# Kernel optimization log

Hardware: AMD Instinct MI355X
Metric: run time of the kernel (lower is better)

## Reference

```python
import jax, jax.numpy as jnp
import numpy as np

N = 100000      # nodes
E = 1_000_000   # edges (avg degree ~10)
D_IN = 64
HID = 64
N_CLS = 32


def setup_inputs() -> dict:
    key = jax.random.key(0)
    ks = jax.random.split(key, 9)
    x = jax.random.normal(ks[0], (N, D_IN), dtype=jnp.float32)
    edge_index = jax.random.randint(ks[1], (2, E), 0, N, dtype=jnp.int32)
    s_in = 1.0 / np.sqrt(D_IN)
    s_h = 1.0 / np.sqrt(HID)
    W1 = jax.random.normal(ks[2], (D_IN, HID), dtype=jnp.float32) * s_in
    b1 = jnp.zeros((HID,), dtype=jnp.float32)
    W2 = jax.random.normal(ks[3], (HID, HID), dtype=jnp.float32) * s_h
    b2 = jnp.zeros((HID,), dtype=jnp.float32)
    Wl = jax.random.normal(ks[4], (HID, N_CLS), dtype=jnp.float32) * s_h
    bl = jnp.zeros((N_CLS,), dtype=jnp.float32)
    return {"x": x, "edge_index": edge_index,
            "W1": W1, "b1": b1, "W2": W2, "b2": b2, "Wl": Wl, "bl": bl}


def reference(x, edge_index, W1, b1, W2, b2, Wl, bl):
    # GCNConv default: add self-loops, symmetric normalization D^-1/2 (A+I) D^-1/2
    loop = jnp.arange(N, dtype=edge_index.dtype)
    src = jnp.concatenate([edge_index[0], loop])  # [E+N]
    dst = jnp.concatenate([edge_index[1], loop])  # [E+N]

    deg = jax.ops.segment_sum(jnp.ones_like(dst, dtype=jnp.float32), dst,
                              num_segments=N)              # [N]
    dinv = jnp.where(deg > 0, jax.lax.rsqrt(deg), 0.0)      # D^-1/2
    norm = dinv[src] * dinv[dst]                            # [E+N]

    def gcn_conv(h, W, b):
        h = h @ W                                           # [N, F_out]
        msg = h[src] * norm[:, None]                        # gather + scale
        return jax.ops.segment_sum(msg, dst, num_segments=N) + b

    h = jax.nn.relu(gcn_conv(x, W1, b1))
    h = jax.nn.relu(gcn_conv(h, W2, b2))
    return h @ Wl + bl
```

## Files before the change

kernel.cpp:

```cpp
#include <hip/hip_runtime.h>
#include <hip/hip_fp16.h>
#include <math.h>


#define TPB    256
#define EBLKS  256
#define BSH    9
#define BNODES (1 << BSH)

__global__ __launch_bounds__(TPB)
void k_p1hist(const int* __restrict__ dst, int* __restrict__ OFS,
              int E, int CH, int NBC) {
    __shared__ int h[512];
    int tid = threadIdx.x, b = blockIdx.x;
    for (int i = tid; i < NBC; i += TPB) h[i] = 0;
    __syncthreads();
    int beg = b * CH, end = min(E, beg + CH);
    if (beg < end) {
        int nfull = (end - beg) & ~3;
        for (int i = beg + tid * 4; i < beg + nfull; i += TPB * 4) {
            int4 d = *(const int4*)&dst[i];
            atomicAdd(&h[d.x >> BSH], 1);
            atomicAdd(&h[d.y >> BSH], 1);
            atomicAdd(&h[d.z >> BSH], 1);
            atomicAdd(&h[d.w >> BSH], 1);
        }
        if (tid < (end - beg) - nfull)
            atomicAdd(&h[dst[beg + nfull + tid] >> BSH], 1);
    }
    __syncthreads();
    for (int c = tid; c < NBC; c += TPB) OFS[c * EBLKS + b] = h[c];
}

__global__ __launch_bounds__(TPB)
void k_scanA(const int* __restrict__ OFS, int* __restrict__ bsum, int total) {
    __shared__ int s[TPB];
    int tid = threadIdx.x;
    int i0  = blockIdx.x * 1024 + tid * 4;
    int t = 0;
#pragma unroll
    for (int k = 0; k < 4; ++k) {
        int i = i0 + k;
        t += (i < total) ? OFS[i] : 0;
    }
    s[tid] = t;
    __syncthreads();
    for (int off = TPB / 2; off > 0; off >>= 1) {
        if (tid < off) s[tid] += s[tid + off];
        __syncthreads();
    }
    if (tid == 0) bsum[blockIdx.x] = s[0];
}

__global__ __launch_bounds__(TPB)
void k_scanC(int* __restrict__ OFS, const int* __restrict__ bsum,
             int NBLK, int total) {
    __shared__ int s[TPB];
    __shared__ int pfx;
    int tid = threadIdx.x;
    if (tid < 64) {
        int v = (tid < NBLK && tid < (int)blockIdx.x) ? bsum[tid] : 0;
#pragma unroll
        for (int off = 1; off < 64; off <<= 1) v += __shfl_xor(v, off);
        if (tid == 0) pfx = v;
    }
    int i0 = blockIdx.x * 1024 + tid * 4;
    int v[4];
#pragma unroll
    for (int k = 0; k < 4; ++k) {
        int i = i0 + k;
        v[k] = (i < total) ? OFS[i] : 0;
    }
    int tsum = v[0] + v[1] + v[2] + v[3];
    s[tid] = tsum;
    __syncthreads();
    for (int off = 1; off < TPB; off <<= 1) {
        int x = (tid >= off) ? s[tid - off] : 0;
        __syncthreads();
        s[tid] += x;
        __syncthreads();
    }
    int base = pfx + (s[tid] - tsum);
#pragma unroll
    for (int k = 0; k < 4; ++k) {
        int i = i0 + k;
        if (i < total) {
            OFS[i] = base;
            base += v[k];
        }
    }
}

__global__ __launch_bounds__(TPB)
void k_p1scatter(const int* __restrict__ src, const int* __restrict__ dst,
                 const int* __restrict__ OFS, int* __restrict__ ebuf,
                 int E, int CH, int NBC) {
    __shared__ int cur[512];
    int tid = threadIdx.x, b = blockIdx.x;
    for (int c = tid; c < NBC; c += TPB) cur[c] = OFS[c * EBLKS + b];
    __syncthreads();
    int beg = b * CH, end = min(E, beg + CH);
    if (beg >= end) return;
    int nfull = (end - beg) & ~3;
    for (int i = beg + tid * 4; i < beg + nfull; i += TPB * 4) {
        int4 s4 = *(const int4*)&src[i];
        int4 d4 = *(const int4*)&dst[i];
        int p0 = atomicAdd(&cur[d4.x >> BSH], 1);
        int p1 = atomicAdd(&cur[d4.y >> BSH], 1);
        int p2 = atomicAdd(&cur[d4.z >> BSH], 1);
        int p3 = atomicAdd(&cur[d4.w >> BSH], 1);
        ebuf[p0] = (s4.x << BSH) | (d4.x & (BNODES - 1));
        ebuf[p1] = (s4.y << BSH) | (d4.y & (BNODES - 1));
        ebuf[p2] = (s4.z << BSH) | (d4.z & (BNODES - 1));
        ebuf[p3] = (s4.w << BSH) | (d4.w & (BNODES - 1));
    }
    if (tid < (end - beg) - nfull) {
        int i = beg + nfull + tid;
        int d = dst[i];
        int p = atomicAdd(&cur[d >> BSH], 1);
        ebuf[p] = (src[i] << BSH) | (d & (BNODES - 1));
    }
}

__global__ __launch_bounds__(TPB)
void k_p2(const int* __restrict__ ebuf, const int* __restrict__ OFS,
          int* __restrict__ row_ptr, float* __restrict__ dinv,
          int* __restrict__ colw, int N, int E, int NBC) {
    __shared__ int cnt[BNODES];
    __shared__ int ofs[BNODES];
    __shared__ int s1[TPB];
    int tid = threadIdx.x, c = blockIdx.x;
    int beg = OFS[c * EBLKS];
    int end = (c == NBC - 1) ? E : OFS[(c + 1) * EBLKS];
    for (int i = tid; i < BNODES; i += TPB) cnt[i] = 0;
    __syncthreads();
    for (int i = beg + tid; i < end; i += TPB)
        atomicAdd(&cnt[ebuf[i] & (BNODES - 1)], 1);
    __syncthreads();
    int a0 = cnt[2 * tid], a1 = cnt[2 * tid + 1];
    int pairsum = a0 + a1;
    s1[tid] = pairsum;
    __syncthreads();
    for (int off = 1; off < TPB; off <<= 1) {
        int x = (tid >= off) ? s1[tid - off] : 0;
        __syncthreads();
        s1[tid] += x;
        __syncthreads();
    }
    int ex = s1[tid] - pairsum;
    int node0 = (c << BSH) + 2 * tid;
    ofs[2 * tid]     = beg + ex;
    ofs[2 * tid + 1] = beg + ex + a0;
    if (node0 < N) {
        row_ptr[node0] = beg + ex;
        dinv[node0]    = rsqrtf((float)(a0 + 1));
    }
    if (node0 + 1 < N) {
        row_ptr[node0 + 1] = beg + ex + a0;
        dinv[node0 + 1]    = rsqrtf((float)(a1 + 1));
    }
    if (c == NBC - 1 && tid == 0) row_ptr[N] = E;
    cnt[2 * tid] = 0;
    cnt[2 * tid + 1] = 0;
    __syncthreads();
    for (int i0 = beg + tid; i0 < end; i0 += TPB * 4) {
        int sv[4], dl[4], pos[4];
        int have = 0;
#pragma unroll
        for (int k = 0; k < 4; ++k) {
            int i = i0 + k * TPB;
            if (i < end) {
                int e = ebuf[i];
                sv[k] = e >> BSH;
                dl[k] = e & (BNODES - 1);
                have = k + 1;
            }
        }
#pragma unroll
        for (int k = 0; k < 4; ++k) {
            if (k < have) {
                int r  = atomicAdd(&cnt[dl[k]], 1);
                pos[k] = ofs[dl[k]] + r;
            }
        }
#pragma unroll
        for (int k = 0; k < 4; ++k)
            if (k < have) colw[pos[k]] = sv[k];
    }
}

template <int F, bool FINAL, bool HIN>
__launch_bounds__(256)
__global__ void k_mm(const void* __restrict__ in, const float* __restrict__ W,
                     const float* __restrict__ bias, const float* __restrict__ dinv,
                     void* __restrict__ out, int n) {
    __shared__ float in_s[64 * 68];
    __shared__ float w_s[64 * F];

    const int tid  = threadIdx.x;
    const int row0 = blockIdx.x * 64;

    for (int i4 = tid; i4 < (64 * F) / 4; i4 += 256)
        ((float4*)w_s)[i4] = ((const float4*)W)[i4];

    if constexpr (HIN) {
        for (int idx = tid; idx < 64 * 8; idx += 256) {
            int r  = idx >> 3;
            int c8 = idx & 7;
            uint4 u = make_uint4(0u, 0u, 0u, 0u);
            if (row0 + r < n)
                u = *(const uint4*)((const __half*)in + (size_t)(row0 + r) * 64 + c8 * 8);
            float2 f0 = __half22float2(*(__half2*)&u.x);
            float2 f1 = __half22float2(*(__half2*)&u.y);
            float2 f2 = __half22float2(*(__half2*)&u.z);
            float2 f3 = __half22float2(*(__half2*)&u.w);
            float* o = &in_s[r * 68 + c8 * 8];
            *(float4*)&o[0] = make_float4(f0.x, f0.y, f1.x, f1.y);
            *(float4*)&o[4] = make_float4(f2.x, f2.y, f3.x, f3.y);
        }
    } else {
        for (int idx = tid; idx < 64 * 16; idx += 256) {
            int r  = idx >> 4;
            int c4 = idx & 15;
            float4 v;
            if (row0 + r < n)
                v = *(const float4*)((const float*)in + (size_t)(row0 + r) * 64 + c4 * 4);
            else
                v = make_float4(0.f, 0.f, 0.f, 0.f);
            *(float4*)&in_s[r * 68 + c4 * 4] = v;
        }
    }
    __syncthreads();

    constexpr int CPT = F / 16;
    const int tx = tid & 15;
    const int ty = tid >> 4;

    float acc[4][CPT];
#pragma unroll
    for (int r = 0; r < 4; ++r)
#pragma unroll
        for (int c = 0; c < CPT; ++c) acc[r][c] = 0.f;

#pragma unroll 4
    for (int k = 0; k < 64; ++k) {
        float b[CPT];
#pragma unroll
        for (int c = 0; c < CPT; ++c) b[c] = w_s[k * F + tx * CPT + c];
#pragma unroll
        for (int r = 0; r < 4; ++r) {
            float a = in_s[(ty * 4 + r) * 68 + k];
#pragma unroll
            for (int c = 0; c < CPT; ++c) acc[r][c] = fmaf(a, b[c], acc[r][c]);
        }
    }

#pragma unroll
    for (int r = 0; r < 4; ++r) {
        int row = row0 + ty * 4 + r;
        if (row >= n) continue;
        if constexpr (FINAL) {
#pragma unroll
            for (int c = 0; c < CPT; ++c) {
                int col = tx * CPT + c;
                ((float*)out)[(size_t)row * F + col] = acc[r][c] + bias[col];
            }
        } else {
            float dd = dinv[row];
            __half2 p0 = __floats2half2_rn(acc[r][0] * dd, acc[r][1] * dd);
            __half2 p1 = __floats2half2_rn(acc[r][2] * dd, acc[r][3] * dd);
            uint2 u = make_uint2(*(unsigned*)&p0, *(unsigned*)&p1);
            *(uint2*)((__half*)out + (size_t)row * 64 + tx * 4) = u;
        }
    }
    if constexpr (!FINAL) {
        if (blockIdx.x == 0 && tid < 16)
            *(uint2*)((__half*)out + (size_t)n * 64 + tid * 4) = make_uint2(0u, 0u);
    }
}

__global__ __launch_bounds__(256)
void k_gather(const int* __restrict__ row_ptr, const int* __restrict__ colw,
              const float* __restrict__ dinv, const float* __restrict__ bias,
              const __half* __restrict__ t, __half* __restrict__ agg, int N) {
    int tid  = threadIdx.x;
    int wv   = tid >> 6;
    int lane = tid & 63;
    int g = lane >> 3;
    int p = lane & 7;
    int d = blockIdx.x * 32 + wv * 8 + g;

    int beg = 0, end = 0;
    if (d < N) { beg = row_ptr[d]; end = row_ptr[d + 1]; }

    float acc[8];
#pragma unroll
    for (int k = 0; k < 8; ++k) acc[k] = 0.f;

    for (int e = beg; e < end; e += 2) {
        int s0 = colw[e];
        int s1 = (e + 1 < end) ? colw[e + 1] : N;
        uint4 a0 = *(const uint4*)(t + (size_t)s0 * 64 + p * 8);
        uint4 a1 = *(const uint4*)(t + (size_t)s1 * 64 + p * 8);
        float2 f;
        f = __half22float2(*(__half2*)&a0.x); acc[0] += f.x; acc[1] += f.y;
        f = __half22float2(*(__half2*)&a0.y); acc[2] += f.x; acc[3] += f.y;
        f = __half22float2(*(__half2*)&a0.z); acc[4] += f.x; acc[5] += f.y;
        f = __half22float2(*(__half2*)&a0.w); acc[6] += f.x; acc[7] += f.y;
        f = __half22float2(*(__half2*)&a1.x); acc[0] += f.x; acc[1] += f.y;
        f = __half22float2(*(__half2*)&a1.y); acc[2] += f.x; acc[3] += f.y;
        f = __half22float2(*(__half2*)&a1.z); acc[4] += f.x; acc[5] += f.y;
        f = __half22float2(*(__half2*)&a1.w); acc[6] += f.x; acc[7] += f.y;
    }

    if (d < N) {
        float dd = dinv[d];
        uint4 a = *(const uint4*)(t + (size_t)d * 64 + p * 8);
        float4 b0 = *(const float4*)&bias[p * 8];
        float4 b1 = *(const float4*)&bias[p * 8 + 4];
        float2 s0 = __half22float2(*(__half2*)&a.x);
        float2 s1 = __half22float2(*(__half2*)&a.y);
        float2 s2 = __half22float2(*(__half2*)&a.z);
        float2 s3 = __half22float2(*(__half2*)&a.w);
        float o0 = fmaxf(fmaf(dd, acc[0] + s0.x, b0.x), 0.f);
        float o1 = fmaxf(fmaf(dd, acc[1] + s0.y, b0.y), 0.f);
        float o2 = fmaxf(fmaf(dd, acc[2] + s1.x, b0.z), 0.f);
        float o3 = fmaxf(fmaf(dd, acc[3] + s1.y, b0.w), 0.f);
        float o4 = fmaxf(fmaf(dd, acc[4] + s2.x, b1.x), 0.f);
        float o5 = fmaxf(fmaf(dd, acc[5] + s2.y, b1.y), 0.f);
        float o6 = fmaxf(fmaf(dd, acc[6] + s3.x, b1.z), 0.f);
        float o7 = fmaxf(fmaf(dd, acc[7] + s3.y, b1.w), 0.f);
        __half2 h0 = __floats2half2_rn(o0, o1);
        __half2 h1 = __floats2half2_rn(o2, o3);
        __half2 h2 = __floats2half2_rn(o4, o5);
        __half2 h3 = __floats2half2_rn(o6, o7);
        uint4 u = make_uint4(*(unsigned*)&h0, *(unsigned*)&h1,
                             *(unsigned*)&h2, *(unsigned*)&h3);
        *(uint4*)(agg + (size_t)d * 64 + p * 8) = u;
    }
}

extern "C" void kernel_launch(void* const* d_in, const int* in_sizes, int n_in,
                              void* d_out, int out_size, void* d_ws, size_t ws_size,
                              hipStream_t stream) {
    const float* x  = (const float*)d_in[0];
    const int*   ei = (const int*)d_in[1];
    const float* W1 = (const float*)d_in[2];
    const float* b1 = (const float*)d_in[3];
    const float* W2 = (const float*)d_in[4];
    const float* b2 = (const float*)d_in[5];
    const float* Wl = (const float*)d_in[6];
    const float* bl = (const float*)d_in[7];
    float*       out = (float*)d_out;

    const int N = in_sizes[0] / 64;
    const int E = in_sizes[1] / 2;
    const int* srcp = ei;
    const int* dstp = ei + E;

    const int NBC   = (N + BNODES - 1) / BNODES;
    const int CH    = (((E + EBLKS - 1) / EBLKS) + 3) & ~3;
    const int total = NBC * EBLKS;
    const int NBLK  = (total + 1023) / 1024;

    char*  ws  = (char*)d_ws;
    size_t off = 0;
    auto alloc = [&](size_t bytes) -> void* {
        void* p = (void*)(ws + off);
        off += (bytes + 255) & ~(size_t)255;
        return p;
    };
    int*    OFS     = (int*)alloc(((size_t)total + 1) * 4);
    int*    bsum    = (int*)alloc((size_t)NBLK * 4);
    int*    ebuf    = (int*)alloc((size_t)E * 4);
    int*    row_ptr = (int*)alloc((size_t)(N + 1) * 4);
    float*  dinv    = (float*)alloc((size_t)N * 4);
    int*    colw    = (int*)alloc((size_t)E * 4);
    __half* t1      = (__half*)alloc((size_t)(N + 1) * 64 * 2);
    __half* agg1    = (__half*)alloc((size_t)N * 64 * 2);
    __half* t2      = t1;
    __half* agg2    = agg1;

    const int nb_mm = (N + 63) / 64;
    const int nb_g  = (N + 31) / 32;

    k_p1hist   <<<EBLKS, TPB, 0, stream>>>(dstp, OFS, E, CH, NBC);
    k_scanA    <<<NBLK,  TPB, 0, stream>>>(OFS, bsum, total);
    k_scanC    <<<NBLK,  TPB, 0, stream>>>(OFS, bsum, NBLK, total);
    k_p1scatter<<<EBLKS, TPB, 0, stream>>>(srcp, dstp, OFS, ebuf, E, CH, NBC);
    k_p2       <<<NBC,   TPB, 0, stream>>>(ebuf, OFS, row_ptr, dinv, colw, N, E, NBC);

    k_mm<64, false, false><<<nb_mm, 256, 0, stream>>>(x, W1, nullptr, dinv, t1, N);
    k_gather<<<nb_g, 256, 0, stream>>>(row_ptr, colw, dinv, b1, t1, agg1, N);

    k_mm<64, false, true><<<nb_mm, 256, 0, stream>>>(agg1, W2, nullptr, dinv, t2, N);
    k_gather<<<nb_g, 256, 0, stream>>>(row_ptr, colw, dinv, b2, t2, agg2, N);

    k_mm<32, true, true><<<nb_mm, 256, 0, stream>>>(agg2, Wl, bl, nullptr, out, N);
}
```

Measured before the change: 209.7 us.

## Degree-sort nodes within buckets for gather load balance and unroll edges by four

k_p2 now builds a per-bucket permutation that orders destination nodes by in-degree (counting sort with 64 bins), and k_gather processes nodes in that order so that the 8 node-groups sharing a wavefront have similar edge counts, cutting divergence from the variable-length edge loops. The gather inner loop is also unrolled from 2 to 4 edges per iteration, giving more independent loads in flight. Costs are an extra perm array, an indirection load per node, scattered output writes, and more padding loads for short rows.

Result: slower. 218.8 us (+4.4%).

```diff
diff --git a/kernel.cpp b/kernel.cpp
--- a/kernel.cpp
+++ b/kernel.cpp
@@ -125,10 +125,13 @@
 __global__ __launch_bounds__(TPB)
 void k_p2(const int* __restrict__ ebuf, const int* __restrict__ OFS,
           int* __restrict__ row_ptr, float* __restrict__ dinv,
-          int* __restrict__ colw, int N, int E, int NBC) {
+          int* __restrict__ colw, int* __restrict__ perm,
+          int N, int E, int NBC) {
     __shared__ int cnt[BNODES];
     __shared__ int ofs[BNODES];
     __shared__ int s1[TPB];
+    __shared__ int dh[64];
+    __shared__ int db[64];
     int tid = threadIdx.x, c = blockIdx.x;
     int beg = OFS[c * EBLKS];
     int end = (c == NBC - 1) ? E : OFS[(c + 1) * EBLKS];
@@ -148,21 +151,43 @@
         __syncthreads();
     }
     int ex = s1[tid] - pairsum;
-    int node0 = (c << BSH) + 2 * tid;
+    int cbase = c << BSH;
+    int node0 = cbase + 2 * tid;
+    bool has0 = node0 < N, has1 = node0 + 1 < N;
     ofs[2 * tid]     = beg + ex;
     ofs[2 * tid + 1] = beg + ex + a0;
-    if (node0 < N) {
+    if (has0) {
         row_ptr[node0] = beg + ex;
         dinv[node0]    = rsqrtf((float)(a0 + 1));
     }
-    if (node0 + 1 < N) {
+    if (has1) {
         row_ptr[node0 + 1] = beg + ex + a0;
         dinv[node0 + 1]    = rsqrtf((float)(a1 + 1));
     }
     if (c == NBC - 1 && tid == 0) row_ptr[N] = E;
+
+    if (tid < 64) dh[tid] = 0;
     cnt[2 * tid] = 0;
     cnt[2 * tid + 1] = 0;
     __syncthreads();
+    int b0 = min(a0, 63), b1 = min(a1, 63);
+    if (has0) atomicAdd(&dh[b0], 1);
+    if (has1) atomicAdd(&dh[b1], 1);
+    __syncthreads();
+    if (tid < 64) {
+        int v = dh[tid];
+        int incl = v;
+#pragma unroll
+        for (int o = 1; o < 64; o <<= 1) {
+            int x = __shfl_up(incl, o);
+            if ((tid & 63) >= o) incl += x;
+        }
+        db[tid] = incl - v;
+    }
+    __syncthreads();
+    if (has0) { int r = atomicAdd(&db[b0], 1); perm[cbase + r] = node0; }
+    if (has1) { int r = atomicAdd(&db[b1], 1); perm[cbase + r] = node0 + 1; }
+
     for (int i0 = beg + tid; i0 < end; i0 += TPB * 4) {
         int sv[4], dl[4], pos[4];
         int have = 0;
@@ -281,6 +306,7 @@
 
 __global__ __launch_bounds__(256)
 void k_gather(const int* __restrict__ row_ptr, const int* __restrict__ colw,
+              const int* __restrict__ perm,
               const float* __restrict__ dinv, const float* __restrict__ bias,
               const __half* __restrict__ t, __half* __restrict__ agg, int N) {
     int tid  = threadIdx.x;
@@ -288,20 +314,28 @@
     int lane = tid & 63;
     int g = lane >> 3;
     int p = lane & 7;
-    int d = blockIdx.x * 32 + wv * 8 + g;
-
-    int beg = 0, end = 0;
-    if (d < N) { beg = row_ptr[d]; end = row_ptr[d + 1]; }
+    int idx = blockIdx.x * 32 + wv * 8 + g;
+
+    int d = 0, beg = 0, end = 0;
+    if (idx < N) {
+        d   = perm[idx];
+        beg = row_ptr[d];
+        end = row_ptr[d + 1];
+    }
 
     float acc[8];
 #pragma unroll
     for (int k = 0; k < 8; ++k) acc[k] = 0.f;
 
-    for (int e = beg; e < end; e += 2) {
+    for (int e = beg; e < end; e += 4) {
         int s0 = colw[e];
         int s1 = (e + 1 < end) ? colw[e + 1] : N;
+        int s2 = (e + 2 < end) ? colw[e + 2] : N;
+        int s3 = (e + 3 < end) ? colw[e + 3] : N;
         uint4 a0 = *(const uint4*)(t + (size_t)s0 * 64 + p * 8);
         uint4 a1 = *(const uint4*)(t + (size_t)s1 * 64 + p * 8);
+        uint4 a2 = *(const uint4*)(t + (size_t)s2 * 64 + p * 8);
+        uint4 a3 = *(const uint4*)(t + (size_t)s3 * 64 + p * 8);
         float2 f;
         f = __half22float2(*(__half2*)&a0.x); acc[0] += f.x; acc[1] += f.y;
         f = __half22float2(*(__half2*)&a0.y); acc[2] += f.x; acc[3] += f.y;
@@ -311,9 +345,17 @@
         f = __half22float2(*(__half2*)&a1.y); acc[2] += f.x; acc[3] += f.y;
         f = __half22float2(*(__half2*)&a1.z); acc[4] += f.x; acc[5] += f.y;
         f = __half22float2(*(__half2*)&a1.w); acc[6] += f.x; acc[7] += f.y;
-    }
-
-    if (d < N) {
+        f = __half22float2(*(__half2*)&a2.x); acc[0] += f.x; acc[1] += f.y;
+        f = __half22float2(*(__half2*)&a2.y); acc[2] += f.x; acc[3] += f.y;
+        f = __half22float2(*(__half2*)&a2.z); acc[4] += f.x; acc[5] += f.y;
+        f = __half22float2(*(__half2*)&a2.w); acc[6] += f.x; acc[7] += f.y;
+        f = __half22float2(*(__half2*)&a3.x); acc[0] += f.x; acc[1] += f.y;
+        f = __half22float2(*(__half2*)&a3.y); acc[2] += f.x; acc[3] += f.y;
+        f = __half22float2(*(__half2*)&a3.z); acc[4] += f.x; acc[5] += f.y;
+        f = __half22float2(*(__half2*)&a3.w); acc[6] += f.x; acc[7] += f.y;
+    }
+
+    if (idx < N) {
         float dd = dinv[d];
         uint4 a = *(const uint4*)(t + (size_t)d * 64 + p * 8);
         float4 b0 = *(const float4*)&bias[p * 8];
@@ -376,6 +418,7 @@
     int*    row_ptr = (int*)alloc((size_t)(N + 1) * 4);
     float*  dinv    = (float*)alloc((size_t)N * 4);
     int*    colw    = (int*)alloc((size_t)E * 4);
+    int*    perm    = (int*)alloc((size_t)N * 4);
     __half* t1      = (__half*)alloc((size_t)(N + 1) * 64 * 2);
     __half* agg1    = (__half*)alloc((size_t)N * 64 * 2);
     __half* t2      = t1;
@@ -388,13 +431,13 @@
     k_scanA    <<<NBLK,  TPB, 0, stream>>>(OFS, bsum, total);
     k_scanC    <<<NBLK,  TPB, 0, stream>>>(OFS, bsum, NBLK, total);
     k_p1scatter<<<EBLKS, TPB, 0, stream>>>(srcp, dstp, OFS, ebuf, E, CH, NBC);
-    k_p2       <<<NBC,   TPB, 0, stream>>>(ebuf, OFS, row_ptr, dinv, colw, N, E, NBC);
+    k_p2       <<<NBC,   TPB, 0, stream>>>(ebuf, OFS, row_ptr, dinv, colw, perm, N, E, NBC);
 
     k_mm<64, false, false><<<nb_mm, 256, 0, stream>>>(x, W1, nullptr, dinv, t1, N);
-    k_gather<<<nb_g, 256, 0, stream>>>(row_ptr, colw, dinv, b1, t1, agg1, N);
+    k_gather<<<nb_g, 256, 0, stream>>>(row_ptr, colw, perm, dinv, b1, t1, agg1, N);
 
     k_mm<64, false, true><<<nb_mm, 256, 0, stream>>>(agg1, W2, nullptr, dinv, t2, N);
-    k_gather<<<nb_g, 256, 0, stream>>>(row_ptr, colw, dinv, b2, t2, agg2, N);
+    k_gather<<<nb_g, 256, 0, stream>>>(row_ptr, colw, perm, dinv, b2, t2, agg2, N);
 
     k_mm<32, true, true><<<nb_mm, 256, 0, stream>>>(agg2, Wl, bl, nullptr, out, N);
 }
```

## Shrink CSR buckets to 128 nodes, widen binning blocks, unroll gather by four

Applied to the files above, without the earlier changes.

The bucket shift drops from 9 to 7, so each counting-sort bucket covers 128 nodes and there are about 782 of them. The histogram and scatter kernels move to 1024 threads with larger shared tables, and the second pass now maps one thread per node. The scan prefix loop is generalised so it works with more than 64 partial sums. The gather loop now issues four neighbour row loads per iteration instead of two, to get more memory requests in flight. In exchange, the second pass leaves half its threads idle, there are more scan blocks, and register pressure in the gather rises.

Result: faster. 201.1 us (-4.1%).

```diff
diff --git a/kernel.cpp b/kernel.cpp
--- a/kernel.cpp
+++ b/kernel.cpp
@@ -4,21 +4,22 @@
 
 
 #define TPB    256
+#define TPB1   1024
 #define EBLKS  256
-#define BSH    9
+#define BSH    7
 #define BNODES (1 << BSH)
 
-__global__ __launch_bounds__(TPB)
+__global__ __launch_bounds__(TPB1)
 void k_p1hist(const int* __restrict__ dst, int* __restrict__ OFS,
               int E, int CH, int NBC) {
-    __shared__ int h[512];
+    __shared__ int h[1024];
     int tid = threadIdx.x, b = blockIdx.x;
-    for (int i = tid; i < NBC; i += TPB) h[i] = 0;
+    h[tid] = 0;
     __syncthreads();
     int beg = b * CH, end = min(E, beg + CH);
     if (beg < end) {
         int nfull = (end - beg) & ~3;
-        for (int i = beg + tid * 4; i < beg + nfull; i += TPB * 4) {
+        for (int i = beg + tid * 4; i < beg + nfull; i += TPB1 * 4) {
             int4 d = *(const int4*)&dst[i];
             atomicAdd(&h[d.x >> BSH], 1);
             atomicAdd(&h[d.y >> BSH], 1);
@@ -29,7 +30,7 @@
             atomicAdd(&h[dst[beg + nfull + tid] >> BSH], 1);
     }
     __syncthreads();
-    for (int c = tid; c < NBC; c += TPB) OFS[c * EBLKS + b] = h[c];
+    for (int c = tid; c < NBC; c += TPB1) OFS[c * EBLKS + b] = h[c];
 }
 
 __global__ __launch_bounds__(TPB)
@@ -53,13 +54,13 @@
 }
 
 __global__ __launch_bounds__(TPB)
-void k_scanC(int* __restrict__ OFS, const int* __restrict__ bsum,
-             int NBLK, int total) {
+void k_scanC(int* __restrict__ OFS, const int* __restrict__ bsum, int total) {
     __shared__ int s[TPB];
     __shared__ int pfx;
     int tid = threadIdx.x;
     if (tid < 64) {
-        int v = (tid < NBLK && tid < (int)blockIdx.x) ? bsum[tid] : 0;
+        int v = 0;
+        for (int j = tid; j < (int)blockIdx.x; j += 64) v += bsum[j];
 #pragma unroll
         for (int off = 1; off < 64; off <<= 1) v += __shfl_xor(v, off);
         if (tid == 0) pfx = v;
@@ -91,18 +92,18 @@
     }
 }
 
-__global__ __launch_bounds__(TPB)
+__global__ __launch_bounds__(TPB1)
 void k_p1scatter(const int* __restrict__ src, const int* __restrict__ dst,
                  const int* __restrict__ OFS, int* __restrict__ ebuf,
                  int E, int CH, int NBC) {
-    __shared__ int cur[512];
+    __shared__ int cur[1024];
     int tid = threadIdx.x, b = blockIdx.x;
-    for (int c = tid; c < NBC; c += TPB) cur[c] = OFS[c * EBLKS + b];
+    for (int c = tid; c < NBC; c += TPB1) cur[c] = OFS[c * EBLKS + b];
     __syncthreads();
     int beg = b * CH, end = min(E, beg + CH);
     if (beg >= end) return;
     int nfull = (end - beg) & ~3;
-    for (int i = beg + tid * 4; i < beg + nfull; i += TPB * 4) {
+    for (int i = beg + tid * 4; i < beg + nfull; i += TPB1 * 4) {
         int4 s4 = *(const int4*)&src[i];
         int4 d4 = *(const int4*)&dst[i];
         int p0 = atomicAdd(&cur[d4.x >> BSH], 1);
@@ -132,14 +133,13 @@
     int tid = threadIdx.x, c = blockIdx.x;
     int beg = OFS[c * EBLKS];
     int end = (c == NBC - 1) ? E : OFS[(c + 1) * EBLKS];
-    for (int i = tid; i < BNODES; i += TPB) cnt[i] = 0;
+    if (tid < BNODES) cnt[tid] = 0;
     __syncthreads();
     for (int i = beg + tid; i < end; i += TPB)
         atomicAdd(&cnt[ebuf[i] & (BNODES - 1)], 1);
     __syncthreads();
-    int a0 = cnt[2 * tid], a1 = cnt[2 * tid + 1];
-    int pairsum = a0 + a1;
-    s1[tid] = pairsum;
+    int a = (tid < BNODES) ? cnt[tid] : 0;
+    s1[tid] = a;
     __syncthreads();
     for (int off = 1; off < TPB; off <<= 1) {
         int x = (tid >= off) ? s1[tid - off] : 0;
@@ -147,21 +147,17 @@
         s1[tid] += x;
         __syncthreads();
     }
-    int ex = s1[tid] - pairsum;
-    int node0 = (c << BSH) + 2 * tid;
-    ofs[2 * tid]     = beg + ex;
-    ofs[2 * tid + 1] = beg + ex + a0;
-    if (node0 < N) {
-        row_ptr[node0] = beg + ex;
-        dinv[node0]    = rsqrtf((float)(a0 + 1));
-    }
-    if (node0 + 1 < N) {
-        row_ptr[node0 + 1] = beg + ex + a0;
-        dinv[node0 + 1]    = rsqrtf((float)(a1 + 1));
+    int ex = s1[tid] - a;
+    if (tid < BNODES) {
+        int node = (c << BSH) + tid;
+        ofs[tid] = beg + ex;
+        if (node < N) {
+            row_ptr[node] = beg + ex;
+            dinv[node]    = rsqrtf((float)(a + 1));
+        }
+        cnt[tid] = 0;
     }
     if (c == NBC - 1 && tid == 0) row_ptr[N] = E;
-    cnt[2 * tid] = 0;
-    cnt[2 * tid + 1] = 0;
     __syncthreads();
     for (int i0 = beg + tid; i0 < end; i0 += TPB * 4) {
         int sv[4], dl[4], pos[4];
@@ -297,11 +293,15 @@
 #pragma unroll
     for (int k = 0; k < 8; ++k) acc[k] = 0.f;
 
-    for (int e = beg; e < end; e += 2) {
+    for (int e = beg; e < end; e += 4) {
         int s0 = colw[e];
         int s1 = (e + 1 < end) ? colw[e + 1] : N;
+        int s2 = (e + 2 < end) ? colw[e + 2] : N;
+        int s3 = (e + 3 < end) ? colw[e + 3] : N;
         uint4 a0 = *(const uint4*)(t + (size_t)s0 * 64 + p * 8);
         uint4 a1 = *(const uint4*)(t + (size_t)s1 * 64 + p * 8);
+        uint4 a2 = *(const uint4*)(t + (size_t)s2 * 64 + p * 8);
+        uint4 a3 = *(const uint4*)(t + (size_t)s3 * 64 + p * 8);
         float2 f;
         f = __half22float2(*(__half2*)&a0.x); acc[0] += f.x; acc[1] += f.y;
         f = __half22float2(*(__half2*)&a0.y); acc[2] += f.x; acc[3] += f.y;
@@ -311,6 +311,14 @@
         f = __half22float2(*(__half2*)&a1.y); acc[2] += f.x; acc[3] += f.y;
         f = __half22float2(*(__half2*)&a1.z); acc[4] += f.x; acc[5] += f.y;
         f = __half22float2(*(__half2*)&a1.w); acc[6] += f.x; acc[7] += f.y;
+        f = __half22float2(*(__half2*)&a2.x); acc[0] += f.x; acc[1] += f.y;
+        f = __half22float2(*(__half2*)&a2.y); acc[2] += f.x; acc[3] += f.y;
+        f = __half22float2(*(__half2*)&a2.z); acc[4] += f.x; acc[5] += f.y;
+        f = __half22float2(*(__half2*)&a2.w); acc[6] += f.x; acc[7] += f.y;
+        f = __half22float2(*(__half2*)&a3.x); acc[0] += f.x; acc[1] += f.y;
+        f = __half22float2(*(__half2*)&a3.y); acc[2] += f.x; acc[3] += f.y;
+        f = __half22float2(*(__half2*)&a3.z); acc[4] += f.x; acc[5] += f.y;
+        f = __half22float2(*(__half2*)&a3.w); acc[6] += f.x; acc[7] += f.y;
     }
 
     if (d < N) {
@@ -384,11 +392,11 @@
     const int nb_mm = (N + 63) / 64;
     const int nb_g  = (N + 31) / 32;
 
-    k_p1hist   <<<EBLKS, TPB, 0, stream>>>(dstp, OFS, E, CH, NBC);
-    k_scanA    <<<NBLK,  TPB, 0, stream>>>(OFS, bsum, total);
-    k_scanC    <<<NBLK,  TPB, 0, stream>>>(OFS, bsum, NBLK, total);
-    k_p1scatter<<<EBLKS, TPB, 0, stream>>>(srcp, dstp, OFS, ebuf, E, CH, NBC);
-    k_p2       <<<NBC,   TPB, 0, stream>>>(ebuf, OFS, row_ptr, dinv, colw, N, E, NBC);
+    k_p1hist   <<<EBLKS, TPB1, 0, stream>>>(dstp, OFS, E, CH, NBC);
+    k_scanA    <<<NBLK,  TPB,  0, stream>>>(OFS, bsum, total);
+    k_scanC    <<<NBLK,  TPB,  0, stream>>>(OFS, bsum, total);
+    k_p1scatter<<<EBLKS, TPB1, 0, stream>>>(srcp, dstp, OFS, ebuf, E, CH, NBC);
+    k_p2       <<<NBC,   TPB,  0, stream>>>(ebuf, OFS, row_ptr, dinv, colw, N, E, NBC);
 
     k_mm<64, false, false><<<nb_mm, 256, 0, stream>>>(x, W1, nullptr, dinv, t1, N);
     k_gather<<<nb_g, 256, 0, stream>>>(row_ptr, colw, dinv, b1, t1, agg1, N);
```
